# Kernel tuning notes

Hardware: AMD Instinct MI355X
Metric: run time of the kernel (lower is better)

The kernel has to match this reference:

```python
import jax, jax.numpy as jnp
from jax import lax
import numpy as np

B, T, IN, H, OUT, FC = 128, 1024, 256, 512, 1, 64


def setup_inputs() -> dict:
    key = jax.random.key(0)
    ks = jax.random.split(key, 16)
    s = 0.05
    inp = {
        "x": jax.random.normal(ks[0], (B, T, IN), dtype=jnp.float32),
        "length_list": jax.random.randint(ks[1], (B,), 1, T),
        # layer 0 LSTM params (PyTorch layout: [4H, in], gate order i,f,g,o)
        "w_ih_l0": jax.random.normal(ks[2], (4 * H, IN), dtype=jnp.float32) * s,
        "w_hh_l0": jax.random.normal(ks[3], (4 * H, H), dtype=jnp.float32) * s,
        "b_ih_l0": jax.random.normal(ks[4], (4 * H,), dtype=jnp.float32) * s,
        "b_hh_l0": jax.random.normal(ks[5], (4 * H,), dtype=jnp.float32) * s,
        # layer 1 LSTM params
        "w_ih_l1": jax.random.normal(ks[6], (4 * H, H), dtype=jnp.float32) * s,
        "w_hh_l1": jax.random.normal(ks[7], (4 * H, H), dtype=jnp.float32) * s,
        "b_ih_l1": jax.random.normal(ks[8], (4 * H,), dtype=jnp.float32) * s,
        "b_hh_l1": jax.random.normal(ks[9], (4 * H,), dtype=jnp.float32) * s,
        # MLP head
        "fc_w": jax.random.normal(ks[10], (FC, H), dtype=jnp.float32) * s,
        "fc_b": jax.random.normal(ks[11], (FC,), dtype=jnp.float32) * s,
        "fc2_w": jax.random.normal(ks[12], (OUT, FC), dtype=jnp.float32) * s,
        "fc2_b": jax.random.normal(ks[13], (OUT,), dtype=jnp.float32) * s,
    }
    return inp


def _lstm_layer(x, w_ih, w_hh, b_ih, b_hh):
    # x: [B, T, D_in] -> hidden sequence [B, T, H]. PyTorch gate order: i, f, g, o.
    bsz = x.shape[0]
    hsz = w_hh.shape[1]
    # input contribution for all timesteps at once: [B, T, 4H]
    xg = jnp.einsum('btd,gd->btg', x, w_ih) + b_ih + b_hh

    def step(carry, xg_t):
        h, c = carry
        g = xg_t + h @ w_hh.T  # [B, 4H]
        i, f, gg, o = jnp.split(g, 4, axis=-1)
        i = jax.nn.sigmoid(i)
        f = jax.nn.sigmoid(f)
        gg = jnp.tanh(gg)
        o = jax.nn.sigmoid(o)
        c = f * c + i * gg
        h = o * jnp.tanh(c)
        return (h, c), h

    h0 = jnp.zeros((bsz, hsz), x.dtype)
    (_, _), hs = lax.scan(step, (h0, h0), jnp.swapaxes(xg, 0, 1))  # hs: [T, B, H]
    return jnp.swapaxes(hs, 0, 1)


def reference(x, length_list, w_ih_l0, w_hh_l0, b_ih_l0, b_hh_l0,
              w_ih_l1, w_hh_l1, b_ih_l1, b_hh_l1, fc_w, fc_b, fc2_w, fc2_b):
    # 2-layer LSTM (batch_first), take last timestep, fc->relu->fc2->sigmoid, squeeze.
    h = _lstm_layer(x, w_ih_l0, w_hh_l0, b_ih_l0, b_hh_l0)
    h = _lstm_layer(h, w_ih_l1, w_hh_l1, b_ih_l1, b_hh_l1)
    last = h[:, -1, :]  # [B, H]
    z = jax.nn.relu(last @ fc_w.T + fc_b)  # [B, 64]
    z = z @ fc2_w.T + fc2_b  # [B, 1]
    return jnp.squeeze(jax.nn.sigmoid(z), axis=1)  # [B]
```

## Files before the change

### kernel.cpp

```cpp
#include <hip/hip_runtime.h>
#include <hip/hip_bf16.h>
#include <stdint.h>

#define Bx  128
#define Tt  1024
#define INx 256
#define Hx  512
#define RB  16
#define RING 8
#define LSTR 520
#define RSLOT (Bx*Hx)

#define HWREG_XCC_ID_ENC (20 | (0 << 6) | (31 << 11))

typedef _Float16 half8 __attribute__((ext_vector_type(8)));
typedef float float4v __attribute__((ext_vector_type(4)));

__device__ __forceinline__ float sigf(float x) { return 1.0f / (1.0f + expf(-x)); }

__device__ __forceinline__ half8 cvt8(const float* __restrict__ p) {
    float4v f0 = *(const float4v*)(p);
    float4v f1 = *(const float4v*)(p + 4);
    half8 a;
    a[0] = (_Float16)f0[0]; a[1] = (_Float16)f0[1];
    a[2] = (_Float16)f0[2]; a[3] = (_Float16)f0[3];
    a[4] = (_Float16)f1[0]; a[5] = (_Float16)f1[1];
    a[6] = (_Float16)f1[2]; a[7] = (_Float16)f1[3];
    return a;
}

__device__ __forceinline__ void vm0() { asm volatile("s_waitcnt vmcnt(0)" ::: "memory"); }

__device__ __forceinline__ void pin(half8& v) { asm volatile("" : "+a"(v)); }

template<bool L2M>
__device__ __forceinline__ half8 ldq(const _Float16* p) {
    half8 v;
    if (L2M) asm volatile("global_load_dwordx4 %0, %1, off sc0"       : "=v"(v) : "v"(p) : "memory");
    else     asm volatile("global_load_dwordx4 %0, %1, off sc0 sc1"   : "=v"(v) : "v"(p) : "memory");
    return v;
}
template<bool L2M>
__device__ __forceinline__ void stw(void* p, unsigned v) {
    if (L2M) asm volatile("global_store_dword %0, %1, off"            :: "v"(p), "v"(v) : "memory");
    else     asm volatile("global_store_dword %0, %1, off sc0 sc1"    :: "v"(p), "v"(v) : "memory");
}

__device__ __forceinline__ unsigned ldctr(const unsigned* p) {
    return __hip_atomic_load(p, __ATOMIC_RELAXED, __HIP_MEMORY_SCOPE_AGENT);
}
__device__ __forceinline__ void stflag(unsigned* p, unsigned v) {
    __hip_atomic_store(p, v, __ATOMIC_RELAXED, __HIP_MEMORY_SCOPE_AGENT);
}

__device__ __forceinline__ void pollge(const unsigned* b0, unsigned t0, int n0,
                                       const unsigned* b1, unsigned t1, int n1, int lane) {
    const unsigned* p = nullptr; unsigned t = 0; int act = 0;
    if (lane < n0)                          { p = b0 + lane;        t = t0; act = 1; }
    else if (lane >= 16 && lane < 16 + n1)  { p = b1 + (lane - 16); t = t1; act = 1; }
    for (;;) {
        int ok = 1;
        if (act) ok = (ldctr(p) >= t);
        if (__all(ok)) break;
        __builtin_amdgcn_s_sleep(1);
    }
}

template<int NC, int NA>
__device__ __forceinline__ void mfma2(const _Float16* buf, int arow, int koff,
                                      const half8 (&B0)[NA], const half8 (&B1)[NA],
                                      float4v& a0, float4v& a1) {
    #pragma unroll
    for (int c = 0; c < NC; ++c) {
        half8 a = *(const half8*)(buf + arow + c * 32 + koff);
        a0 = __builtin_amdgcn_mfma_f32_16x16x32_f16(a, B0[c], a0, 0, 0, 0);
        a1 = __builtin_amdgcn_mfma_f32_16x16x32_f16(a, B1[c], a1, 0, 0, 0);
    }
}

__global__ void zero_ctr(unsigned* __restrict__ p) {
    for (int i = threadIdx.x; i < 1024; i += 512)
        __hip_atomic_store(&p[i], 0u, __ATOMIC_RELAXED, __HIP_MEMORY_SCOPE_AGENT);
}

template<bool L2M>
__device__ void run_lstm(
    int g, int id, int tid,
    const float* __restrict__ x,
    const float* __restrict__ w_ih_l0, const float* __restrict__ w_hh_l0,
    const float* __restrict__ b_ih_l0, const float* __restrict__ b_hh_l0,
    const float* __restrict__ w_ih_l1, const float* __restrict__ w_hh_l1,
    const float* __restrict__ b_ih_l1, const float* __restrict__ b_hh_l1,
    unsigned* __restrict__ syncw, _Float16* __restrict__ h0r, _Float16* __restrict__ h1r,
    _Float16* bufX, _Float16* bufH, float (*gbuf)[RB][33])
{
    const int L   = id & 1;
    const int ub  = id >> 1;
    const int u0  = ub * 32;
    const int grow = g * RB;

    const int wv   = tid >> 6;
    const int lane = tid & 63;
    const int n    = lane & 15;
    const int quad = lane >> 4;
    const int koff = quad * 8;
    const int arow = n * LSTR;
    const int srow = tid >> 4;
    const int sc   = tid & 15;

    unsigned* flags = syncw + 512;
    unsigned* fl0 = flags + g * 32;
    unsigned* fl1 = flags + g * 32 + 16;
    unsigned* myf = flags + g * 32 + L * 16 + ub;

    const float* bi = L ? b_ih_l1 : b_ih_l0;
    const float* bh = L ? b_hh_l1 : b_hh_l0;
    float bias[4][2];
    #pragma unroll
    for (int q = 0; q < 4; ++q)
        #pragma unroll
        for (int j = 0; j < 2; ++j) {
            int u = q * Hx + u0 + 2 * sc + j;
            bias[q][j] = bi[u] + bh[u];
        }

    float cs0 = 0.0f, cs1 = 0.0f;

    if (L == 0) {
        half8 W1a[8], W1b[8], W2a[16], W2b[16];
        const int wrA = wv * Hx + u0 + n, wrB = wrA + 16;
        #pragma unroll
        for (int c = 0; c < 8; ++c) {
            W1a[c] = cvt8(w_ih_l0 + (size_t)wrA * INx + c * 32 + koff);
            W1b[c] = cvt8(w_ih_l0 + (size_t)wrB * INx + c * 32 + koff);
        }
        #pragma unroll
        for (int c = 0; c < 16; ++c) {
            W2a[c] = cvt8(w_hh_l0 + (size_t)wrA * Hx + c * 32 + koff);
            W2b[c] = cvt8(w_hh_l0 + (size_t)wrB * Hx + c * 32 + koff);
        }
        #pragma unroll
        for (int c = 0; c < 8; ++c)  { pin(W1a[c]); pin(W1b[c]); }
        #pragma unroll
        for (int c = 0; c < 16; ++c) { pin(W2a[c]); pin(W2b[c]); }

        for (int s = 0; s < Tt; ++s) {
            {
                const float* xp = x + ((size_t)(grow + srow) * Tt + s) * INx + sc * 16;
                float4v x0 = *(const float4v*)(xp);
                float4v x1 = *(const float4v*)(xp + 4);
                float4v x2 = *(const float4v*)(xp + 8);
                float4v x3 = *(const float4v*)(xp + 12);
                half8 hA, hB;
                hA[0]=(_Float16)x0[0]; hA[1]=(_Float16)x0[1]; hA[2]=(_Float16)x0[2]; hA[3]=(_Float16)x0[3];
                hA[4]=(_Float16)x1[0]; hA[5]=(_Float16)x1[1]; hA[6]=(_Float16)x1[2]; hA[7]=(_Float16)x1[3];
                hB[0]=(_Float16)x2[0]; hB[1]=(_Float16)x2[1]; hB[2]=(_Float16)x2[2]; hB[3]=(_Float16)x2[3];
                hB[4]=(_Float16)x3[0]; hB[5]=(_Float16)x3[1]; hB[6]=(_Float16)x3[2]; hB[7]=(_Float16)x3[3];
                *(half8*)(bufX + srow * LSTR + sc * 16)     = hA;
                *(half8*)(bufX + srow * LSTR + sc * 16 + 8) = hB;
            }
            __syncthreads();
            float4v a0 = {0.f,0.f,0.f,0.f}, a1 = {0.f,0.f,0.f,0.f};
            if (wv != 0) {
                mfma2<8>(bufX, arow, koff, W1a, W1b, a0, a1);
            } else {
                int n0 = (s > 0) ? 16 : 0;
                int n1 = (((s & 3) == 0) && s >= 8) ? 16 : 0;
                pollge(fl0, (unsigned)s, n0, fl1, (unsigned)(s - 4), n1, lane);
            }
            __syncthreads();
            if (s > 0) {
                const _Float16* hp = h0r + (size_t)((s - 1) & 7) * RSLOT
                                   + (size_t)(grow + srow) * Hx + sc * 32;
                half8 v0 = ldq<L2M>(hp), v1 = ldq<L2M>(hp + 8),
                      v2 = ldq<L2M>(hp + 16), v3 = ldq<L2M>(hp + 24);
                if (wv == 0) mfma2<8>(bufX, arow, koff, W1a, W1b, a0, a1);
                vm0();
                *(half8*)(bufH + srow * LSTR + sc * 32)      = v0;
                *(half8*)(bufH + srow * LSTR + sc * 32 + 8)  = v1;
                *(half8*)(bufH + srow * LSTR + sc * 32 + 16) = v2;
                *(half8*)(bufH + srow * LSTR + sc * 32 + 24) = v3;
                __syncthreads();
                mfma2<16>(bufH, arow, koff, W2a, W2b, a0, a1);
            } else if (wv == 0) {
                mfma2<8>(bufX, arow, koff, W1a, W1b, a0, a1);
            }
            #pragma unroll
            for (int r = 0; r < 4; ++r) {
                gbuf[wv][quad * 4 + r][n]      = a0[r];
                gbuf[wv][quad * 4 + r][16 + n] = a1[r];
            }
            __syncthreads();
            {
                unsigned pv = 0;
                #pragma unroll
                for (int j = 0; j < 2; ++j) {
                    float iv = gbuf[0][srow][2 * sc + j] + bias[0][j];
                    float fv = gbuf[1][srow][2 * sc + j] + bias[1][j];
                    float gv = gbuf[2][srow][2 * sc + j] + bias[2][j];
                    float ov = gbuf[3][srow][2 * sc + j] + bias[3][j];
                    float& cc = j ? cs1 : cs0;
                    float cn = sigf(fv) * cc + sigf(iv) * tanhf(gv);
                    cc = cn;
                    _Float16 hn = (_Float16)(sigf(ov) * tanhf(cn));
                    pv |= (unsigned)__builtin_bit_cast(unsigned short, hn) << (16 * j);
                }
                stw<L2M>(h0r + (size_t)(s & 7) * RSLOT + (size_t)(grow + srow) * Hx + u0 + 2 * sc, pv);
            }
            vm0();
            __syncthreads();
            if (tid == 0) stflag(myf, (unsigned)(s + 1));
        }
    } else {
        half8 W1a[16], W1b[16], W2a[16], W2b[16];
        const int wrA = wv * Hx + u0 + n, wrB = wrA + 16;
        #pragma unroll
        for (int c = 0; c < 16; ++c) {
            W1a[c] = cvt8(w_ih_l1 + (size_t)wrA * Hx + c * 32 + koff);
            W1b[c] = cvt8(w_ih_l1 + (size_t)wrB * Hx + c * 32 + koff);
            W2a[c] = cvt8(w_hh_l1 + (size_t)wrA * Hx + c * 32 + koff);
            W2b[c] = cvt8(w_hh_l1 + (size_t)wrB * Hx + c * 32 + koff);
        }
        #pragma unroll
        for (int c = 0; c < 16; ++c) {
            pin(W1a[c]); pin(W1b[c]); pin(W2a[c]); pin(W2b[c]);
        }

        for (int s = 0; s < Tt; ++s) {
            if (wv == 0) pollge(fl0, (unsigned)(s + 1), 16, nullptr, 0u, 0, lane);
            __syncthreads();
            {
                const _Float16* hp0 = h0r + (size_t)(s & 7) * RSLOT
                                    + (size_t)(grow + srow) * Hx + sc * 32;
                half8 v0 = ldq<L2M>(hp0), v1 = ldq<L2M>(hp0 + 8),
                      v2 = ldq<L2M>(hp0 + 16), v3 = ldq<L2M>(hp0 + 24);
                vm0();
                *(half8*)(bufX + srow * LSTR + sc * 32)      = v0;
                *(half8*)(bufX + srow * LSTR + sc * 32 + 8)  = v1;
                *(half8*)(bufX + srow * LSTR + sc * 32 + 16) = v2;
                *(half8*)(bufX + srow * LSTR + sc * 32 + 24) = v3;
            }
            __syncthreads();
            float4v a0 = {0.f,0.f,0.f,0.f}, a1 = {0.f,0.f,0.f,0.f};
            if (wv != 0) {
                mfma2<16>(bufX, arow, koff, W1a, W1b, a0, a1);
            } else if (s > 0) {
                pollge(fl1, (unsigned)s, 16, nullptr, 0u, 0, lane);
            }
            __syncthreads();
            if (s > 0) {
                const _Float16* hp1 = h1r + (size_t)((s - 1) & 7) * RSLOT
                                    + (size_t)(grow + srow) * Hx + sc * 32;
                half8 w0 = ldq<L2M>(hp1), w1 = ldq<L2M>(hp1 + 8),
                      w2 = ldq<L2M>(hp1 + 16), w3 = ldq<L2M>(hp1 + 24);
                if (wv == 0) mfma2<16>(bufX, arow, koff, W1a, W1b, a0, a1);
                vm0();
                *(half8*)(bufH + srow * LSTR + sc * 32)      = w0;
                *(half8*)(bufH + srow * LSTR + sc * 32 + 8)  = w1;
                *(half8*)(bufH + srow * LSTR + sc * 32 + 16) = w2;
                *(half8*)(bufH + srow * LSTR + sc * 32 + 24) = w3;
                __syncthreads();
                mfma2<16>(bufH, arow, koff, W2a, W2b, a0, a1);
            } else if (wv == 0) {
                mfma2<16>(bufX, arow, koff, W1a, W1b, a0, a1);
            }
            #pragma unroll
            for (int r = 0; r < 4; ++r) {
                gbuf[wv][quad * 4 + r][n]      = a0[r];
                gbuf[wv][quad * 4 + r][16 + n] = a1[r];
            }
            __syncthreads();
            {
                unsigned pv = 0;
                #pragma unroll
                for (int j = 0; j < 2; ++j) {
                    float iv = gbuf[0][srow][2 * sc + j] + bias[0][j];
                    float fv = gbuf[1][srow][2 * sc + j] + bias[1][j];
                    float gv = gbuf[2][srow][2 * sc + j] + bias[2][j];
                    float ov = gbuf[3][srow][2 * sc + j] + bias[3][j];
                    float& cc = j ? cs1 : cs0;
                    float cn = sigf(fv) * cc + sigf(iv) * tanhf(gv);
                    cc = cn;
                    _Float16 hn = (_Float16)(sigf(ov) * tanhf(cn));
                    pv |= (unsigned)__builtin_bit_cast(unsigned short, hn) << (16 * j);
                }
                _Float16* dst = h1r + (size_t)(s & 7) * RSLOT + (size_t)(grow + srow) * Hx + u0 + 2 * sc;
                if (s == Tt - 1) stw<false>(dst, pv);
                else             stw<L2M>(dst, pv);
            }
            vm0();
            __syncthreads();
            if (tid == 0) stflag(myf, (unsigned)(s + 1));
        }
    }
}

__global__ __launch_bounds__(256, 1) void lstm_persist(
    const float* __restrict__ x,
    const float* __restrict__ w_ih_l0, const float* __restrict__ w_hh_l0,
    const float* __restrict__ b_ih_l0, const float* __restrict__ b_hh_l0,
    const float* __restrict__ w_ih_l1, const float* __restrict__ w_hh_l1,
    const float* __restrict__ b_ih_l1, const float* __restrict__ b_hh_l1,
    unsigned* __restrict__ syncw,
    _Float16* __restrict__ h0r, _Float16* __restrict__ h1r)
{
    __shared__ _Float16 bufX[RB * LSTR];
    __shared__ _Float16 bufH[RB * LSTR];
    __shared__ float gbuf[4][RB][33];
    __shared__ unsigned smap[256];
    __shared__ int sh_g, sh_id, sh_valid;

    const int tid = threadIdx.x;
    const int blk = blockIdx.x;

    const unsigned xcc = (unsigned)__builtin_amdgcn_s_getreg(HWREG_XCC_ID_ENC) & 7u;

    if (tid == 0) {
        __hip_atomic_store(&syncw[32 + blk], xcc, __ATOMIC_RELAXED, __HIP_MEMORY_SCOPE_AGENT);
        __hip_atomic_fetch_add(&syncw[0], 1u, __ATOMIC_RELEASE, __HIP_MEMORY_SCOPE_AGENT);
        while (__hip_atomic_load(&syncw[0], __ATOMIC_ACQUIRE, __HIP_MEMORY_SCOPE_AGENT) < 256u)
            __builtin_amdgcn_s_sleep(2);
    }
    __syncthreads();
    smap[tid] = __hip_atomic_load(&syncw[32 + tid], __ATOMIC_RELAXED, __HIP_MEMORY_SCOPE_AGENT);
    __syncthreads();
    if (tid == 0) {
        int cnt[8] = {0,0,0,0,0,0,0,0};
        int rank = 0;
        for (int i = 0; i < 256; ++i) {
            int m = (int)(smap[i] & 7u);
            cnt[m]++;
            if (i < blk && m == (int)xcc) rank++;
        }
        int ok = 1;
        #pragma unroll
        for (int i = 0; i < 8; ++i) ok &= (cnt[i] == 32);
        sh_valid = ok;
        sh_g  = ok ? (int)xcc : (blk >> 5);
        sh_id = ok ? rank : (blk & 31);
    }
    __syncthreads();

    if (sh_valid)
        run_lstm<true >(sh_g, sh_id, tid, x, w_ih_l0, w_hh_l0, b_ih_l0, b_hh_l0,
                        w_ih_l1, w_hh_l1, b_ih_l1, b_hh_l1, syncw, h0r, h1r,
                        bufX, bufH, gbuf);
    else
        run_lstm<false>(sh_g, sh_id, tid, x, w_ih_l0, w_hh_l0, b_ih_l0, b_hh_l0,
                        w_ih_l1, w_hh_l1, b_ih_l1, b_hh_l1, syncw, h0r, h1r,
                        bufX, bufH, gbuf);
}

__global__ __launch_bounds__(64) void fc_kernel(
    const _Float16* __restrict__ h1,
    const float* __restrict__ fc_w, const float* __restrict__ fc_b,
    const float* __restrict__ fc2_w, const float* __restrict__ fc2_b,
    float* __restrict__ out)
{
    const int b = blockIdx.x;
    const int j = threadIdx.x;
    const _Float16* h = h1 + (size_t)b * Hx;
    const float* w = fc_w + (size_t)j * Hx;
    float acc = fc_b[j];
    for (int k = 0; k < Hx; k += 2) {
        unsigned pv = __hip_atomic_load((const unsigned*)(h + k),
                                        __ATOMIC_RELAXED, __HIP_MEMORY_SCOPE_AGENT);
        _Float16 lo = __builtin_bit_cast(_Float16, (unsigned short)(pv & 0xffffu));
        _Float16 hi = __builtin_bit_cast(_Float16, (unsigned short)(pv >> 16));
        acc += (float)lo * w[k] + (float)hi * w[k + 1];
    }
    float p = fmaxf(acc, 0.0f) * fc2_w[j];
    #pragma unroll
    for (int off = 32; off; off >>= 1) p += __shfl_down(p, off);
    if (j == 0) out[b] = 1.0f / (1.0f + expf(-(p + fc2_b[0])));
}

extern "C" void kernel_launch(void* const* d_in, const int* in_sizes, int n_in,
                              void* d_out, int out_size, void* d_ws, size_t ws_size,
                              hipStream_t stream) {
    const float* x       = (const float*)d_in[0];
    const float* w_ih_l0 = (const float*)d_in[2];
    const float* w_hh_l0 = (const float*)d_in[3];
    const float* b_ih_l0 = (const float*)d_in[4];
    const float* b_hh_l0 = (const float*)d_in[5];
    const float* w_ih_l1 = (const float*)d_in[6];
    const float* w_hh_l1 = (const float*)d_in[7];
    const float* b_ih_l1 = (const float*)d_in[8];
    const float* b_hh_l1 = (const float*)d_in[9];
    const float* fc_w    = (const float*)d_in[10];
    const float* fc_b    = (const float*)d_in[11];
    const float* fc2_w   = (const float*)d_in[12];
    const float* fc2_b   = (const float*)d_in[13];
    float* out = (float*)d_out;

    char* ws = (char*)d_ws;
    unsigned* syncw = (unsigned*)ws;
    _Float16* h0r = (_Float16*)(ws + 4096);
    _Float16* h1r = (_Float16*)(ws + 4096 + RING * RSLOT * sizeof(_Float16));

    zero_ctr<<<1, 512, 0, stream>>>(syncw);
    lstm_persist<<<256, 256, 0, stream>>>(x,
        w_ih_l0, w_hh_l0, b_ih_l0, b_hh_l0,
        w_ih_l1, w_hh_l1, b_ih_l1, b_hh_l1,
        syncw, h0r, h1r);
    fc_kernel<<<Bx, 64, 0, stream>>>(h1r + 7 * RSLOT, fc_w, fc_b, fc2_w, fc2_b, out);
}
```

Baseline: 4.571 ms.

## Use cache-scoped flag loads/stores and prefetch next x timestep in layer 0

Replaces the agent-scope atomic flag load and store with inline-asm global loads and stores carrying explicit cache-policy bits. When all cooperating blocks share an XCC (L2M), polls alternate between L2-scoped and MALL-scoped reads, and flag stores skip the sc0 sc1 bits. Separately, layer 0 now issues the next timestep's x loads right after the barrier, so they are in flight while the gate computation runs. The aim is lower cross-block handoff latency on the recurrent critical path, at the cost of relying on hand-picked cache-coherence bits for correctness.

```diff
diff --git a/kernel.cpp b/kernel.cpp
--- a/kernel.cpp
+++ b/kernel.cpp
@@ -46,22 +46,39 @@
     else     asm volatile("global_store_dword %0, %1, off sc0 sc1"    :: "v"(p), "v"(v) : "memory");
 }
 
-__device__ __forceinline__ unsigned ldctr(const unsigned* p) {
-    return __hip_atomic_load(p, __ATOMIC_RELAXED, __HIP_MEMORY_SCOPE_AGENT);
-}
+__device__ __forceinline__ unsigned ldf_l2(const unsigned* p) {
+    unsigned v;
+    asm volatile("global_load_dword %0, %1, off sc0\n\ts_waitcnt vmcnt(0)"
+                 : "=v"(v) : "v"(p) : "memory");
+    return v;
+}
+__device__ __forceinline__ unsigned ldf_mall(const unsigned* p) {
+    unsigned v;
+    asm volatile("global_load_dword %0, %1, off sc0 sc1\n\ts_waitcnt vmcnt(0)"
+                 : "=v"(v) : "v"(p) : "memory");
+    return v;
+}
+template<bool L2M>
 __device__ __forceinline__ void stflag(unsigned* p, unsigned v) {
-    __hip_atomic_store(p, v, __ATOMIC_RELAXED, __HIP_MEMORY_SCOPE_AGENT);
-}
-
+    if (L2M) asm volatile("global_store_dword %0, %1, off"         :: "v"(p), "v"(v) : "memory");
+    else     asm volatile("global_store_dword %0, %1, off sc0 sc1" :: "v"(p), "v"(v) : "memory");
+}
+
+template<bool L2M>
 __device__ __forceinline__ void pollge(const unsigned* b0, unsigned t0, int n0,
                                        const unsigned* b1, unsigned t1, int n1, int lane) {
     const unsigned* p = nullptr; unsigned t = 0; int act = 0;
     if (lane < n0)                          { p = b0 + lane;        t = t0; act = 1; }
     else if (lane >= 16 && lane < 16 + n1)  { p = b1 + (lane - 16); t = t1; act = 1; }
+    unsigned it = 0;
     for (;;) {
         int ok = 1;
-        if (act) ok = (ldctr(p) >= t);
+        if (act) {
+            unsigned v = (L2M && !(it & 1)) ? ldf_l2(p) : ldf_mall(p);
+            ok = (v >= t);
+        }
         if (__all(ok)) break;
+        ++it;
         __builtin_amdgcn_s_sleep(1);
     }
 }
@@ -144,29 +161,37 @@
         #pragma unroll
         for (int c = 0; c < 16; ++c) { pin(W2a[c]); pin(W2b[c]); }
 
+        const float* xrp = x + ((size_t)(grow + srow) * Tt) * INx + sc * 16;
+        float4v xr0 = *(const float4v*)(xrp);
+        float4v xr1 = *(const float4v*)(xrp + 4);
+        float4v xr2 = *(const float4v*)(xrp + 8);
+        float4v xr3 = *(const float4v*)(xrp + 12);
+
         for (int s = 0; s < Tt; ++s) {
             {
-                const float* xp = x + ((size_t)(grow + srow) * Tt + s) * INx + sc * 16;
-                float4v x0 = *(const float4v*)(xp);
-                float4v x1 = *(const float4v*)(xp + 4);
-                float4v x2 = *(const float4v*)(xp + 8);
-                float4v x3 = *(const float4v*)(xp + 12);
                 half8 hA, hB;
-                hA[0]=(_Float16)x0[0]; hA[1]=(_Float16)x0[1]; hA[2]=(_Float16)x0[2]; hA[3]=(_Float16)x0[3];
-                hA[4]=(_Float16)x1[0]; hA[5]=(_Float16)x1[1]; hA[6]=(_Float16)x1[2]; hA[7]=(_Float16)x1[3];
-                hB[0]=(_Float16)x2[0]; hB[1]=(_Float16)x2[1]; hB[2]=(_Float16)x2[2]; hB[3]=(_Float16)x2[3];
-                hB[4]=(_Float16)x3[0]; hB[5]=(_Float16)x3[1]; hB[6]=(_Float16)x3[2]; hB[7]=(_Float16)x3[3];
+                hA[0]=(_Float16)xr0[0]; hA[1]=(_Float16)xr0[1]; hA[2]=(_Float16)xr0[2]; hA[3]=(_Float16)xr0[3];
+                hA[4]=(_Float16)xr1[0]; hA[5]=(_Float16)xr1[1]; hA[6]=(_Float16)xr1[2]; hA[7]=(_Float16)xr1[3];
+                hB[0]=(_Float16)xr2[0]; hB[1]=(_Float16)xr2[1]; hB[2]=(_Float16)xr2[2]; hB[3]=(_Float16)xr2[3];
+                hB[4]=(_Float16)xr3[0]; hB[5]=(_Float16)xr3[1]; hB[6]=(_Float16)xr3[2]; hB[7]=(_Float16)xr3[3];
                 *(half8*)(bufX + srow * LSTR + sc * 16)     = hA;
                 *(half8*)(bufX + srow * LSTR + sc * 16 + 8) = hB;
             }
             __syncthreads();
+            if (s + 1 < Tt) {
+                const float* xp = xrp + (size_t)(s + 1) * INx;
+                xr0 = *(const float4v*)(xp);
+                xr1 = *(const float4v*)(xp + 4);
+                xr2 = *(const float4v*)(xp + 8);
+                xr3 = *(const float4v*)(xp + 12);
+            }
             float4v a0 = {0.f,0.f,0.f,0.f}, a1 = {0.f,0.f,0.f,0.f};
             if (wv != 0) {
                 mfma2<8>(bufX, arow, koff, W1a, W1b, a0, a1);
             } else {
                 int n0 = (s > 0) ? 16 : 0;
                 int n1 = (((s & 3) == 0) && s >= 8) ? 16 : 0;
-                pollge(fl0, (unsigned)s, n0, fl1, (unsigned)(s - 4), n1, lane);
+                pollge<L2M>(fl0, (unsigned)s, n0, fl1, (unsigned)(s - 4), n1, lane);
             }
             __syncthreads();
             if (s > 0) {
@@ -209,7 +234,7 @@
             }
             vm0();
             __syncthreads();
-            if (tid == 0) stflag(myf, (unsigned)(s + 1));
+            if (tid == 0) stflag<L2M>(myf, (unsigned)(s + 1));
         }
     } else {
         half8 W1a[16], W1b[16], W2a[16], W2b[16];
@@ -227,7 +252,7 @@
         }
 
         for (int s = 0; s < Tt; ++s) {
-            if (wv == 0) pollge(fl0, (unsigned)(s + 1), 16, nullptr, 0u, 0, lane);
+            if (wv == 0) pollge<L2M>(fl0, (unsigned)(s + 1), 16, nullptr, 0u, 0, lane);
             __syncthreads();
             {
                 const _Float16* hp0 = h0r + (size_t)(s & 7) * RSLOT
@@ -245,7 +270,7 @@
             if (wv != 0) {
                 mfma2<16>(bufX, arow, koff, W1a, W1b, a0, a1);
             } else if (s > 0) {
-                pollge(fl1, (unsigned)s, 16, nullptr, 0u, 0, lane);
+                pollge<L2M>(fl1, (unsigned)s, 16, nullptr, 0u, 0, lane);
             }
             __syncthreads();
             if (s > 0) {
@@ -290,7 +315,7 @@
             }
             vm0();
             __syncthreads();
-            if (tid == 0) stflag(myf, (unsigned)(s + 1));
+            if (tid == 0) stflag<L2M>(myf, (unsigned)(s + 1));
         }
     }
 }
```

After: 3.734 ms. 1.22x faster.
